# Optimization experiments

Measured on AMD Instinct MI355X. Metric: run time of the kernel, lower is better.

Reference implementation:

```python
import jax, jax.numpy as jnp
import numpy as np
from itertools import product

SPATIAL1 = (41, 1600, 1408)  # (z,y,x) = grid[::-1] + [1,0,0]
NUM_BATCH = 2
BN_EPS = 1e-3

# ---------- numpy rulebook construction (spconv-style, done once on host) ----------

def _encode(c, shape):
    D, H, W = [int(v) for v in shape]
    return ((c[:, 0].astype(np.int64) * D + c[:, 1]) * H + c[:, 2]) * W + c[:, 3]

def _lookup(skeys, order, cand):
    pos = np.clip(np.searchsorted(skeys, cand), 0, len(skeys) - 1)
    hit = skeys[pos] == cand
    return hit, order[pos]

def _pad_rb(pairs, n_in, n_out):
    P = max(max(len(a) for a, _ in pairs), 1)
    K = len(pairs)
    ii = np.full((K, P), n_in, np.int32)   # sentinel -> zero feature row
    oo = np.full((K, P), n_out, np.int32)  # sentinel -> dummy output row
    for k, (a, b) in enumerate(pairs):
        ii[k, :len(a)] = a
        oo[k, :len(b)] = b
    return ii, oo

def _subm_rb(coords, shape):
    # SubMConv3d k=3 p=1 s=1: output sites == input sites
    N = len(coords)
    keys = _encode(coords, shape)
    order = np.argsort(keys); skeys = keys[order]
    dims = np.array(shape)
    pairs = []
    for off in product((-1, 0, 1), repeat=3):
        nb = coords[:, 1:] + np.array(off)
        ok = (nb >= 0).all(1) & (nb < dims).all(1)
        oid = np.nonzero(ok)[0]
        cand = _encode(np.concatenate([coords[ok, :1], nb[ok]], 1), shape)
        hit, iid = _lookup(skeys, order, cand)
        pairs.append((iid[hit].astype(np.int32), oid[hit].astype(np.int32)))
    return _pad_rb(pairs, N, N)

def _down_rb(coords, in_shape, ks, st, pd):
    # SparseConv3d: output site active iff any kernel tap hits an active input
    dims = np.array(in_shape); ks = np.array(ks); st = np.array(st); pd = np.array(pd)
    out_shape = (dims + 2 * pd - ks) // st + 1
    offs = list(product(*[range(int(k)) for k in ks]))
    outs = []
    for off in offs:
        o = coords[:, 1:] + pd - np.array(off)
        ok = (o % st == 0).all(1)
        od = o // st
        ok &= (od >= 0).all(1) & (od < out_shape).all(1)
        outs.append(np.concatenate([coords[ok, :1], od[ok]], 1))
    out_coords = np.unique(np.concatenate(outs, 0), axis=0)
    keys = _encode(coords, in_shape)
    order = np.argsort(keys); skeys = keys[order]
    pairs = []
    for off in offs:
        ic = out_coords[:, 1:] * st - pd + np.array(off)
        ok = (ic >= 0).all(1) & (ic < dims).all(1)
        oid = np.nonzero(ok)[0]
        cand = _encode(np.concatenate([out_coords[ok, :1], ic[ok]], 1), in_shape)
        hit, iid = _lookup(skeys, order, cand)
        pairs.append((iid[hit].astype(np.int32), oid[hit].astype(np.int32)))
    ii, oo = _pad_rb(pairs, len(coords), len(out_coords))
    return ii, oo, out_coords, tuple(int(v) for v in out_shape)

def _gen_coords(rng):
    # clustered LiDAR-like active voxels (surfaces -> local density)
    D, H, W = SPATIAL1
    per = []
    for b in range(NUM_BATCH):
        centers = rng.integers([3, 30, 30], [D - 4, H - 31, W - 31], size=(600, 3))
        pts = centers[:, None, :] + rng.integers(-3, 4, size=(600, 60, 3))
        pts = np.clip(pts.reshape(-1, 3), 0, np.array([D - 1, H - 1, W - 1]))
        uniq = np.unique(pts, axis=0)
        per.append(np.concatenate([np.full((len(uniq), 1), b, np.int64), uniq], 1))
    return np.concatenate(per, 0)

CHANS = [(27, 4, 16), (27, 16, 16), (27, 16, 32), (27, 32, 32), (27, 32, 32),
         (27, 32, 64), (27, 64, 64), (27, 64, 64), (27, 64, 64), (27, 64, 64),
         (27, 64, 64), (3, 64, 128)]

def setup_inputs() -> dict:
    rng = np.random.default_rng(0)
    coords = _gen_coords(rng)  # (N,4) [b,z,y,x]
    N = len(coords)
    s1i, s1o = _subm_rb(coords, SPATIAL1)
    d2i, d2o, c2, s2 = _down_rb(coords, SPATIAL1, (3, 3, 3), (2, 2, 2), (1, 1, 1))
    s2i, s2o = _subm_rb(c2, s2)
    d3i, d3o, c3, s3 = _down_rb(c2, s2, (3, 3, 3), (2, 2, 2), (1, 1, 1))
    s3i, s3o = _subm_rb(c3, s3)
    d4i, d4o, c4, s4 = _down_rb(c3, s3, (3, 3, 3), (2, 2, 2), (0, 1, 1))
    s4i, s4o = _subm_rb(c4, s4)
    oi, oo, c5, s5 = _down_rb(c4, s4, (3, 1, 1), (2, 1, 1), (0, 0, 0))

    key = jax.random.key(0)
    ks = jax.random.split(key, 40)
    inp = {}
    for i, (K, ci, co) in enumerate(CHANS):
        inp[f"w{i}"] = (jax.random.normal(ks[i], (K, ci, co), jnp.float32)
                         / np.sqrt(K * ci)).astype(jnp.float32)
        kb = jax.random.split(ks[12 + i], 4)
        inp[f"bn{i}"] = jnp.stack([
            jax.random.uniform(kb[0], (co,)) + 0.5,   # gamma
            jax.random.normal(kb[1], (co,)) * 0.1,    # beta
            jax.random.normal(kb[2], (co,)) * 0.1,    # running mean
            jax.random.uniform(kb[3], (co,)) + 0.5,   # running var
        ]).astype(jnp.float32)
    inp["voxels"] = jax.random.normal(ks[30], (N, 5, 4), jnp.float32)
    inp["voxel_num_points"] = jax.random.randint(ks[31], (N,), 0, 6).astype(jnp.int32)
    for name, arr in [("subm1_in", s1i), ("subm1_out", s1o), ("down2_in", d2i),
                      ("down2_out", d2o), ("subm2_in", s2i), ("subm2_out", s2o),
                      ("down3_in", d3i), ("down3_out", d3o), ("subm3_in", s3i),
                      ("subm3_out", s3o), ("down4_in", d4i), ("down4_out", d4o),
                      ("subm4_in", s4i), ("subm4_out", s4o), ("out_in", oi),
                      ("out_out", oo)]:
        inp[name] = jnp.asarray(arr)
    inp["batch_idx"] = jnp.asarray(c5[:, 0].astype(np.int32))
    inp["n2"] = len(c2); inp["n3"] = len(c3); inp["n4"] = len(c4); inp["n5"] = len(c5)
    inp["n_batch"] = NUM_BATCH
    return inp

# ---------- jax forward ----------

def _sconv(feats, w, in_idx, out_idx, n_out):
    # gather -> per-kernel-offset GEMM -> scatter-add (spconv implicit GEMM)
    fpad = jnp.concatenate([feats, jnp.zeros((1, feats.shape[1]), feats.dtype)], 0)
    g = fpad[in_idx]                                  # (K,P,Cin)
    contrib = jnp.einsum('kpi,kio->kpo', g, w)        # (K,P,Cout)
    out = jnp.zeros((n_out + 1, w.shape[2]), feats.dtype)
    return out.at[out_idx].add(contrib)[:n_out]

def _bnrelu(x, bn):
    g, b, m, v = bn  # eval-mode BatchNorm1d, eps=1e-3
    return jax.nn.relu((x - m) * jax.lax.rsqrt(v + BN_EPS) * g + b)

def reference(voxels, voxel_num_points, w0, w1, w2, w3, w4, w5, w6, w7, w8, w9,
              w10, w11, bn0, bn1, bn2, bn3, bn4, bn5, bn6, bn7, bn8, bn9, bn10,
              bn11, subm1_in, subm1_out, down2_in, down2_out, subm2_in, subm2_out,
              down3_in, down3_out, subm3_in, subm3_out, down4_in, down4_out,
              subm4_in, subm4_out, out_in, out_out, batch_idx, n2, n3, n4, n5,
              n_batch):
    # mean-VFE: average point features per voxel
    denom = jnp.maximum(voxel_num_points.astype(voxels.dtype), 1.0)[:, None]
    x = voxels.sum(1) / denom                              # (N,4)
    n1 = x.shape[0]
    x = _bnrelu(_sconv(x, w0, subm1_in, subm1_out, n1), bn0)   # conv_input
    x = _bnrelu(_sconv(x, w1, subm1_in, subm1_out, n1), bn1)   # conv1
    x = _bnrelu(_sconv(x, w2, down2_in, down2_out, n2), bn2)   # conv2 (s2)
    x = _bnrelu(_sconv(x, w3, subm2_in, subm2_out, n2), bn3)
    x = _bnrelu(_sconv(x, w4, subm2_in, subm2_out, n2), bn4)
    x = _bnrelu(_sconv(x, w5, down3_in, down3_out, n3), bn5)   # conv3 (s2)
    x = _bnrelu(_sconv(x, w6, subm3_in, subm3_out, n3), bn6)
    x = _bnrelu(_sconv(x, w7, subm3_in, subm3_out, n3), bn7)
    x = _bnrelu(_sconv(x, w8, down4_in, down4_out, n4), bn8)   # conv4 (s2)
    x = _bnrelu(_sconv(x, w9, subm4_in, subm4_out, n4), bn9)
    x = _bnrelu(_sconv(x, w10, subm4_in, subm4_out, n4), bn10)
    x = _bnrelu(_sconv(x, w11, out_in, out_out, n5), bn11)     # conv_out
    # dc_feats: per-sample global max pool over active voxels (== max_pool1d)
    dc = jax.ops.segment_max(x, batch_idx, num_segments=n_batch)
    return dc
```

## Files before the change

### kernel.cpp

```cpp
#include <hip/hip_runtime.h>

#define TPB 256
typedef unsigned short u16;
typedef __attribute__((ext_vector_type(8))) short short8v;
typedef __attribute__((ext_vector_type(4))) float f32x4;

__device__ __forceinline__ u16 f2bf(float x) {
    unsigned u = __float_as_uint(x);
    return (u16)((u + 0x7FFFu + ((u >> 16) & 1u)) >> 16);
}
__device__ __forceinline__ float bf2f(u16 h) {
    return __uint_as_float(((unsigned)h) << 16);
}

template<int CS>
__device__ __forceinline__ int swzc(int r, int c) {
    constexpr int PH = (CS == 8) ? 0 : 1;
    return c ^ ((r >> PH) & (CS - 1));
}

__device__ __forceinline__ int xcd_swz(int bid, int nwg) {
    int q = nwg >> 3, r = nwg & 7;
    int x = bid & 7, idx = bid >> 3;
    return (x < r ? x * (q + 1) : r * (q + 1) + (x - r) * q) + idx;
}

__device__ __forceinline__ void gld16(const u16* g, u16* l) {
    __builtin_amdgcn_global_load_lds(
        (const __attribute__((address_space(1))) void*)g,
        (__attribute__((address_space(3))) void*)l, 16, 0, 0);
}

__global__ void vfe_kernel(const float* __restrict__ voxels,
                           const int* __restrict__ nump,
                           float* __restrict__ x, int N) {
    int i = blockIdx.x * blockDim.x + threadIdx.x;
    if (i >= N * 4) return;
    int n = i >> 2, c = i & 3;
    const float* v = voxels + (long)n * 20 + c;
    float s = v[0] + v[4] + v[8] + v[12] + v[16];
    x[i] = s / fmaxf((float)nump[n], 1.0f);
}

__global__ void inv_build_kernel(const int* __restrict__ rb_in,
                                 const int* __restrict__ rb_out,
                                 int* __restrict__ inv,
                                 int KP, int P, int K, int n_in) {
    int t = blockIdx.x * blockDim.x + threadIdx.x;
    if (t >= KP) return;
    int ii = rb_in[t];
    if (ii == n_in) return;
    int k = t / P;
    inv[(long)rb_out[t] * K + k] = ii;
}

struct WPE { const float* w; u16* oh; u16* ol; int K, ci, co, total; };
struct WPA { WPE e[9]; };
__global__ void wprep_kernel(WPA a, int grand) {
    int t = blockIdx.x * blockDim.x + threadIdx.x;
    if (t >= grand) return;
    #pragma unroll
    for (int i = 0; i < 9; ++i) {
        if (t < a.e[i].total) {
            const WPE& E = a.e[i];
            int cc = E.ci * E.co;
            int k = t / cc, r = t % cc, c = r / E.co, o = r % E.co;
            float x = E.w[t];
            u16 h = f2bf(x);
            float lf = x - bf2f(h);
            int cs = E.ci >> 3, ph = (cs == 8) ? 0 : 1;
            int ch = c >> 3, e = c & 7;
            int sch = ch ^ ((o >> ph) & (cs - 1));
            long d = ((long)k * E.co + o) * E.ci + sch * 8 + e;
            E.oh[d] = h; E.ol[d] = f2bf(lf);
            return;
        }
        t -= a.e[i].total;
    }
}

__global__ void wprep_paired_kernel(const float* __restrict__ w,
                                    u16* __restrict__ oh, u16* __restrict__ ol,
                                    int co, int total) {
    int t = blockIdx.x * blockDim.x + threadIdx.x;
    if (t >= total) return;
    int p = t / (co * 32);
    int rem = t % (co * 32);
    int o = rem / 32, ci = rem % 32;
    int tap = 2 * p + (ci >> 4);
    float x = (tap < 27) ? w[((long)tap * 16 + (ci & 15)) * co + o] : 0.f;
    u16 h = f2bf(x);
    float lf = x - bf2f(h);
    int ch = ci >> 3, e = ci & 7;
    int sch = ch ^ ((o >> 1) & 3);
    long d = ((long)p * co + o) * 32 + sch * 8 + e;
    oh[d] = h; ol[d] = f2bf(lf);
}

template<int CO, int K>
__global__ __launch_bounds__(256)
void dconv4_kernel(const float* __restrict__ feats,
                   const float* __restrict__ w,
                   const float* __restrict__ bn,
                   const int* __restrict__ inv,
                   u16* __restrict__ oh, u16* __restrict__ ol,
                   int n_out) {
    constexpr int OG = CO / 4;
    __shared__ float sW[K * 4 * CO];
    for (int i = threadIdx.x; i < K * 4 * CO; i += 256) sW[i] = w[i];
    __syncthreads();
    long t = (long)blockIdx.x * 256 + threadIdx.x;
    int row = (int)(t / OG), og = (int)(t % OG);
    if (row >= n_out) return;
    float a0 = 0.f, a1 = 0.f, a2 = 0.f, a3 = 0.f;
    for (int k = 0; k < K; ++k) {
        int idx = inv[(long)row * K + k];
        if (idx < 0) continue;
        float4 av = *(const float4*)(feats + (long)idx * 4);
        const float* wk = sW + k * 4 * CO + og * 4;
        #pragma unroll
        for (int ci = 0; ci < 4; ++ci) {
            float a = (&av.x)[ci];
            a0 = fmaf(a, wk[ci * CO + 0], a0);
            a1 = fmaf(a, wk[ci * CO + 1], a1);
            a2 = fmaf(a, wk[ci * CO + 2], a2);
            a3 = fmaf(a, wk[ci * CO + 3], a3);
        }
    }
    float4 g = *(const float4*)(bn + og * 4);
    float4 b = *(const float4*)(bn + CO + og * 4);
    float4 m = *(const float4*)(bn + 2 * CO + og * 4);
    float4 v = *(const float4*)(bn + 3 * CO + og * 4);
    float o4[4];
    o4[0] = fmaxf((a0 - m.x) * rsqrtf(v.x + 1e-3f) * g.x + b.x, 0.f);
    o4[1] = fmaxf((a1 - m.y) * rsqrtf(v.y + 1e-3f) * g.y + b.y, 0.f);
    o4[2] = fmaxf((a2 - m.z) * rsqrtf(v.z + 1e-3f) * g.z + b.z, 0.f);
    o4[3] = fmaxf((a3 - m.w) * rsqrtf(v.w + 1e-3f) * g.w + b.w, 0.f);
    long base = (long)row * CO + og * 4;
    #pragma unroll
    for (int c = 0; c < 4; ++c) {
        u16 h = f2bf(o4[c]);
        oh[base + c] = h;
        ol[base + c] = f2bf(o4[c] - bf2f(h));
    }
}

template<int CI, int CO, int KP, int KT, bool PAIRED>
__global__ __launch_bounds__(256, 4)
void mconv_kernel(const u16* __restrict__ fh, const u16* __restrict__ fl,
                  const u16* __restrict__ wh, const u16* __restrict__ wl,
                  const int* __restrict__ inv,
                  const u16* __restrict__ zpage,
                  float* __restrict__ part, long slab_elems,
                  int n_out, int kpb) {
    constexpr int CS  = CI / 8;
    constexpr int LCS = (CS == 8) ? 3 : 2;
    constexpr int PH  = (CS == 8) ? 0 : 1;
    constexpr int KS  = CI / 32;
    constexpr int WC  = (CO >= 32) ? 2 : 1;
    constexpr int MT  = (WC == 2) ? 2 : 1;
    constexpr int NTW = CO / (16 * WC);
    constexpr int ASL = 64 * CS;
    constexpr int BSL = CO * CS;
    constexpr int AIT = (ASL + 255) / 256;
    constexpr int BIT = (BSL + 255) / 256;

    __shared__ __align__(16) u16 sAh[64 * CI];
    __shared__ __align__(16) u16 sAl[64 * CI];
    __shared__ __align__(16) u16 sBh[CO * CI];
    __shared__ __align__(16) u16 sBl[CO * CI];
    __shared__ int sI[64 * KT];

    const int t = threadIdx.x;
    const int bx = xcd_swz(blockIdx.x, gridDim.x);
    const int brow = bx * 64;
    const int kbeg = blockIdx.y * kpb;
    const int kend = (kbeg + kpb < KP) ? (kbeg + kpb) : KP;

    const int lane = t & 63, wid = t >> 6;
    const int wr = wid / WC, wc = wid % WC;
    const int frow = lane & 15;
    const int fch  = lane >> 4;

    {
        long base = (long)brow * KT, lim = (long)n_out * KT;
        for (int i = t; i < 64 * KT; i += 256)
            sI[i] = (base + i < lim) ? inv[base + i] : -1;
    }

    f32x4 acc[MT][NTW];
    #pragma unroll
    for (int mt = 0; mt < MT; ++mt)
        #pragma unroll
        for (int nt = 0; nt < NTW; ++nt) {
            acc[mt][nt][0] = 0.f; acc[mt][nt][1] = 0.f;
            acc[mt][nt][2] = 0.f; acc[mt][nt][3] = 0.f;
        }

    __syncthreads();
    for (int k = kbeg; k < kend; ++k) {
        #pragma unroll
        for (int s = 0; s < AIT; ++s) {
            int slot = s * 256 + t;
            if (ASL % 256 == 0 || slot < ASL) {
                int r = slot >> LCS, cc = slot & (CS - 1);
                int c = cc ^ ((r >> PH) & (CS - 1));
                const u16 *srcH, *srcL;
                if (PAIRED) {
                    int tap = 2 * k + (c >> 1);
                    int idx = (tap < KT) ? sI[r * KT + tap] : -1;
                    srcH = (idx >= 0) ? fh + (long)idx * 16 + (c & 1) * 8 : zpage;
                    srcL = (idx >= 0) ? fl + (long)idx * 16 + (c & 1) * 8 : zpage;
                } else {
                    int idx = sI[r * KT + k];
                    srcH = (idx >= 0) ? fh + (long)idx * CI + c * 8 : zpage;
                    srcL = (idx >= 0) ? fl + (long)idx * CI + c * 8 : zpage;
                }
                gld16(srcH, sAh + (s * 256 + wid * 64) * 8);
                gld16(srcL, sAl + (s * 256 + wid * 64) * 8);
            }
        }
        {
            const u16* gbh = wh + (long)k * CO * CI;
            const u16* gbl = wl + (long)k * CO * CI;
            #pragma unroll
            for (int s = 0; s < BIT; ++s) {
                int slot = s * 256 + t;
                if (BSL % 256 == 0 || slot < BSL) {
                    gld16(gbh + (long)slot * 8, sBh + (s * 256 + wid * 64) * 8);
                    gld16(gbl + (long)slot * 8, sBl + (s * 256 + wid * 64) * 8);
                }
            }
        }
        __syncthreads();

        #pragma unroll
        for (int ks = 0; ks < KS; ++ks) {
            int c = ks * 4 + fch;
            short8v ah[MT], al[MT];
            #pragma unroll
            for (int mt = 0; mt < MT; ++mt) {
                int r = wr * (MT * 16) + mt * 16 + frow;
                int o = r * CI + swzc<CS>(r, c) * 8;
                ah[mt] = *(const short8v*)(sAh + o);
                al[mt] = *(const short8v*)(sAl + o);
            }
            #pragma unroll
            for (int nt = 0; nt < NTW; ++nt) {
                int col = wc * (CO / WC) + nt * 16 + frow;
                int o = col * CI + swzc<CS>(col, c) * 8;
                short8v bh = *(const short8v*)(sBh + o);
                short8v bl = *(const short8v*)(sBl + o);
                #pragma unroll
                for (int mt = 0; mt < MT; ++mt) {
                    acc[mt][nt] = __builtin_amdgcn_mfma_f32_16x16x32_bf16(ah[mt], bh, acc[mt][nt], 0, 0, 0);
                    acc[mt][nt] = __builtin_amdgcn_mfma_f32_16x16x32_bf16(ah[mt], bl, acc[mt][nt], 0, 0, 0);
                    acc[mt][nt] = __builtin_amdgcn_mfma_f32_16x16x32_bf16(al[mt], bh, acc[mt][nt], 0, 0, 0);
                }
            }
        }
        if (k + 1 < kend) __syncthreads();
    }

    float* dst = part + (long)blockIdx.y * slab_elems;
    #pragma unroll
    for (int mt = 0; mt < MT; ++mt) {
        int orow0 = brow + wr * (MT * 16) + mt * 16 + (lane >> 4) * 4;
        #pragma unroll
        for (int nt = 0; nt < NTW; ++nt) {
            int ocol = wc * (CO / WC) + nt * 16 + (lane & 15);
            #pragma unroll
            for (int j = 0; j < 4; ++j) {
                int r = orow0 + j;
                if (r < n_out) dst[(long)r * CO + ocol] = acc[mt][nt][j];
            }
        }
    }
}

template<bool EMIT16>
__global__ void reduce_bnrelu_kernel(const float* __restrict__ part, long stride,
                                     int ys, const float* __restrict__ bn, int co,
                                     float* __restrict__ outf,
                                     u16* __restrict__ oh, u16* __restrict__ ol,
                                     long total) {
    long t = (long)blockIdx.x * blockDim.x + threadIdx.x;
    if (t >= total) return;
    float s = 0.f;
    for (int y = 0; y < ys; ++y) s += part[(long)y * stride + t];
    int o = (int)(t % co);
    float g = bn[o], b = bn[co + o], m = bn[2 * co + o], v = bn[3 * co + o];
    float yv = fmaxf((s - m) * rsqrtf(v + 1e-3f) * g + b, 0.f);
    if (EMIT16) {
        u16 h = f2bf(yv);
        oh[t] = h;
        ol[t] = f2bf(yv - bf2f(h));
    } else {
        outf[t] = yv;
    }
}

__global__ void segmax_kernel(const float* __restrict__ x,
                              const int* __restrict__ bidx,
                              float* __restrict__ out, int rows, int nb) {
    __shared__ float sM[8 * 128];
    for (int i = threadIdx.x; i < nb * 128; i += 256) sM[i] = 0.f;
    __syncthreads();
    int c = threadIdx.x & 127;
    int sub = threadIdx.x >> 7;
    for (int r = blockIdx.x * 2 + sub; r < rows; r += gridDim.x * 2) {
        float v = x[(long)r * 128 + c];
        int b = bidx[r];
        atomicMax((int*)&sM[b * 128 + c], __float_as_int(v));
    }
    __syncthreads();
    for (int i = threadIdx.x; i < nb * 128; i += 256)
        atomicMax((int*)out + i, __float_as_int(sM[i]));
}

extern "C" void kernel_launch(void* const* d_in, const int* in_sizes, int n_in,
                              void* d_out, int out_size, void* d_ws, size_t ws_size,
                              hipStream_t stream) {
    (void)n_in;
    const float* voxels = (const float*)d_in[24];
    const int*   nump   = (const int*)d_in[25];
    const int N  = in_sizes[25];
    const int n2 = in_sizes[30] / 27;
    const int n3 = in_sizes[34] / 27;
    const int n4 = in_sizes[38] / 27;
    const int n5 = in_sizes[42];

    struct L { int wi, rb, K, ci, co, nin, nout; };
    const L layers[12] = {
        {0,  26, 27,  4,  16, N,  N }, {1,  26, 27, 16,  16, N,  N },
        {2,  28, 27, 16,  32, N,  n2}, {3,  30, 27, 32,  32, n2, n2},
        {4,  30, 27, 32,  32, n2, n2}, {5,  32, 27, 32,  64, n2, n3},
        {6,  34, 27, 64,  64, n3, n3}, {7,  34, 27, 64,  64, n3, n3},
        {8,  36, 27, 64,  64, n3, n4}, {9,  38, 27, 64,  64, n4, n4},
        {10, 38, 27, 64,  64, n4, n4}, {11, 40,  3, 64, 128, n4, n5},
    };

    size_t inv_elems = 0, feat_elems = (size_t)N * 4, wt_elems = 0;
    for (int i = 0; i < 12; ++i) {
        size_t ie = (size_t)layers[i].nout * layers[i].K;
        size_t fe = (size_t)layers[i].nout * layers[i].co;
        if (ie > inv_elems)  inv_elems  = ie;
        if (fe > feat_elems) feat_elems = fe;
        if (i >= 3) wt_elems += (size_t)layers[i].K * layers[i].ci * layers[i].co;
    }
    const size_t wp1_elems = 14 * 32 * 16;
    const size_t wp2_elems = 14 * 32 * 32;
    auto al = [](size_t x) { return (x + 255) & ~(size_t)255; };
    char* p = (char*)d_ws;
    u16*   zpage = (u16*)p; p += 256;
    int*   inv  = (int*)p;   p += al(inv_elems * 4);
    float* bufA = (float*)p; p += al(feat_elems * 4);
    u16* ph[2]; u16* pl[2];
    ph[0] = (u16*)p; p += al(feat_elems * 2);
    pl[0] = (u16*)p; p += al(feat_elems * 2);
    ph[1] = (u16*)p; p += al(feat_elems * 2);
    pl[1] = (u16*)p; p += al(feat_elems * 2);
    u16* wth = (u16*)p; p += al(wt_elems * 2);
    u16* wtl = (u16*)p; p += al(wt_elems * 2);
    u16* wp1h = (u16*)p; p += al(wp1_elems * 2);
    u16* wp1l = (u16*)p; p += al(wp1_elems * 2);
    u16* wp2h = (u16*)p; p += al(wp2_elems * 2);
    u16* wp2l = (u16*)p; p += al(wp2_elems * 2);
    float* slab = (float*)p;
    size_t slab_budget = ws_size - (size_t)((char*)slab - (char*)d_ws);

    hipMemsetAsync(zpage, 0, 256, stream);

    {
        long tot = (long)N * 4;
        vfe_kernel<<<dim3((unsigned)((tot + TPB - 1) / TPB)), dim3(TPB), 0, stream>>>(
            voxels, nump, bufA, N);
    }

    size_t woff[9];
    {
        WPA wa;
        size_t off = 0;
        for (int i = 0; i < 9; ++i) {
            const L& l = layers[i + 3];
            woff[i] = off;
            wa.e[i].w  = (const float*)d_in[2 * l.wi];
            wa.e[i].oh = wth + off;
            wa.e[i].ol = wtl + off;
            wa.e[i].K = l.K; wa.e[i].ci = l.ci; wa.e[i].co = l.co;
            wa.e[i].total = l.K * l.ci * l.co;
            off += (size_t)wa.e[i].total;
        }
        int grand = (int)off;
        wprep_kernel<<<dim3((grand + TPB - 1) / TPB), dim3(TPB), 0, stream>>>(wa, grand);
        wprep_paired_kernel<<<dim3(((int)wp1_elems + TPB - 1) / TPB), dim3(TPB), 0, stream>>>(
            (const float*)d_in[2], wp1h, wp1l, 16, (int)wp1_elems);
        wprep_paired_kernel<<<dim3(((int)wp2_elems + TPB - 1) / TPB), dim3(TPB), 0, stream>>>(
            (const float*)d_in[4], wp2h, wp2l, 32, (int)wp2_elems);
    }

    int prev_rb = -1;
    auto build_inv = [&](const L& l) {
        if (l.rb == prev_rb) return;
        const int* rin  = (const int*)d_in[l.rb];
        const int* rout = (const int*)d_in[l.rb + 1];
        int P  = in_sizes[l.rb] / l.K;
        int KP = l.K * P;
        hipMemsetAsync(inv, 0xFF, (size_t)l.nout * l.K * sizeof(int), stream);
        inv_build_kernel<<<dim3((KP + TPB - 1) / TPB), dim3(TPB), 0, stream>>>(
            rin, rout, inv, KP, P, l.K, l.nin);
        prev_rb = l.rb;
    };

    auto pick_ys = [&](unsigned blocks, int ys_max, size_t per) {
        int ys = 1;
        while (ys < ys_max && blocks * (unsigned)ys < 768) ys *= 3;
        if (ys > ys_max) ys = ys_max;
        while (ys > 1 && (size_t)ys * per > slab_budget) ys /= 3;
        return ys;
    };

    {
        const L& l = layers[0];
        build_inv(l);
        long tot = (long)l.nout * 4;
        dconv4_kernel<16, 27><<<dim3((unsigned)((tot + 255) / 256)), 256, 0, stream>>>(
            bufA, (const float*)d_in[0], (const float*)d_in[1], inv,
            ph[0], pl[0], l.nout);
    }

    int cset = 0;
    for (int i = 1; i < 3; ++i) {
        const L& l = layers[i];
        build_inv(l);
        unsigned blocks = (unsigned)((l.nout + 63) / 64);
        size_t per = (size_t)l.nout * l.co * 4;
        int ys = pick_ys(blocks, 3, per);
        int kpb = (14 + ys - 1) / ys;
        long slab_elems = (long)l.nout * l.co;
        dim3 grid(blocks, (unsigned)ys);
        if (i == 1)
            mconv_kernel<32, 16, 14, 27, true><<<grid, 256, 0, stream>>>(
                ph[cset], pl[cset], wp1h, wp1l, inv, zpage,
                slab, slab_elems, l.nout, kpb);
        else
            mconv_kernel<32, 32, 14, 27, true><<<grid, 256, 0, stream>>>(
                ph[cset], pl[cset], wp2h, wp2l, inv, zpage,
                slab, slab_elems, l.nout, kpb);
        long total = (long)l.nout * l.co;
        unsigned rblocks = (unsigned)((total + TPB - 1) / TPB);
        reduce_bnrelu_kernel<true><<<dim3(rblocks), dim3(TPB), 0, stream>>>(
            slab, slab_elems, ys, (const float*)d_in[2 * l.wi + 1], l.co,
            nullptr, ph[cset ^ 1], pl[cset ^ 1], total);
        cset ^= 1;
    }

    for (int i = 3; i < 12; ++i) {
        const L& l = layers[i];
        build_inv(l);
        unsigned blocks = (unsigned)((l.nout + 63) / 64);
        size_t per = (size_t)l.nout * l.co * 4;
        int ys = pick_ys(blocks, (l.K == 27) ? 27 : 3, per);
        int kpb = (l.K + ys - 1) / ys;
        long slab_elems = (long)l.nout * l.co;
        dim3 grid(blocks, (unsigned)ys);
        const u16* fh = ph[cset];
        const u16* fl = pl[cset];
        const u16* whp = wth + woff[i - 3];
        const u16* wlp = wtl + woff[i - 3];

        switch (i) {
        case 3: case 4:
            mconv_kernel<32, 32, 27, 27, false><<<grid, 256, 0, stream>>>(
                fh, fl, whp, wlp, inv, zpage, slab, slab_elems, l.nout, kpb); break;
        case 5:
            mconv_kernel<32, 64, 27, 27, false><<<grid, 256, 0, stream>>>(
                fh, fl, whp, wlp, inv, zpage, slab, slab_elems, l.nout, kpb); break;
        case 11:
            mconv_kernel<64, 128, 3, 3, false><<<grid, 256, 0, stream>>>(
                fh, fl, whp, wlp, inv, zpage, slab, slab_elems, l.nout, kpb); break;
        default:
            mconv_kernel<64, 64, 27, 27, false><<<grid, 256, 0, stream>>>(
                fh, fl, whp, wlp, inv, zpage, slab, slab_elems, l.nout, kpb); break;
        }

        long total = (long)l.nout * l.co;
        unsigned rblocks = (unsigned)((total + TPB - 1) / TPB);
        const float* bn = (const float*)d_in[2 * l.wi + 1];
        if (i < 11) {
            reduce_bnrelu_kernel<true><<<dim3(rblocks), dim3(TPB), 0, stream>>>(
                slab, slab_elems, ys, bn, l.co,
                nullptr, ph[cset ^ 1], pl[cset ^ 1], total);
            cset ^= 1;
        } else {
            reduce_bnrelu_kernel<false><<<dim3(rblocks), dim3(TPB), 0, stream>>>(
                slab, slab_elems, ys, bn, l.co, bufA, nullptr, nullptr, total);
        }
    }

    hipMemsetAsync(d_out, 0, (size_t)out_size * sizeof(float), stream);
    const int* bidx = (const int*)d_in[42];
    int nb = out_size / 128;
    segmax_kernel<<<dim3(128), dim3(256), 0, stream>>>(bufA, bidx, (float*)d_out, n5, nb);
}
```

Measured before the change: 473.3 us.

## Double-buffer sparse conv staging, fuse BN-ReLU epilogue, prebuild all rulebook inverses

The gather-GEMM kernel gets optional double-buffered LDS staging, so the next tap's gather overlaps the current tap's MFMA work. When no K-split is used, it applies BN+ReLU in the epilogue and writes bf16 hi/lo or fp32 output directly, skipping the reduce kernel. All eight inverse rulebooks are now built up front into one arena instead of per layer. The K-split cap for the paired layers rises from 3 to 9. Double buffering doubles LDS use, which may reduce occupancy for the larger-channel layers.

```diff
diff --git a/kernel.cpp b/kernel.cpp
--- a/kernel.cpp
+++ b/kernel.cpp
@@ -145,13 +145,16 @@
     }
 }
 
-template<int CI, int CO, int KP, int KT, bool PAIRED>
+template<int CI, int CO, int KPt, int KT, bool PAIRED, bool DBUF, int EPI>
 __global__ __launch_bounds__(256, 4)
 void mconv_kernel(const u16* __restrict__ fh, const u16* __restrict__ fl,
                   const u16* __restrict__ wh, const u16* __restrict__ wl,
                   const int* __restrict__ inv,
                   const u16* __restrict__ zpage,
                   float* __restrict__ part, long slab_elems,
+                  const float* __restrict__ bn,
+                  u16* __restrict__ oh, u16* __restrict__ ol,
+                  float* __restrict__ outf,
                   int n_out, int kpb) {
     constexpr int CS  = CI / 8;
     constexpr int LCS = (CS == 8) ? 3 : 2;
@@ -164,18 +167,19 @@
     constexpr int BSL = CO * CS;
     constexpr int AIT = (ASL + 255) / 256;
     constexpr int BIT = (BSL + 255) / 256;
-
-    __shared__ __align__(16) u16 sAh[64 * CI];
-    __shared__ __align__(16) u16 sAl[64 * CI];
-    __shared__ __align__(16) u16 sBh[CO * CI];
-    __shared__ __align__(16) u16 sBl[CO * CI];
+    constexpr int NB  = DBUF ? 2 : 1;
+
+    __shared__ __align__(16) u16 sAh[NB][64 * CI];
+    __shared__ __align__(16) u16 sAl[NB][64 * CI];
+    __shared__ __align__(16) u16 sBh[NB][CO * CI];
+    __shared__ __align__(16) u16 sBl[NB][CO * CI];
     __shared__ int sI[64 * KT];
 
     const int t = threadIdx.x;
     const int bx = xcd_swz(blockIdx.x, gridDim.x);
     const int brow = bx * 64;
     const int kbeg = blockIdx.y * kpb;
-    const int kend = (kbeg + kpb < KP) ? (kbeg + kpb) : KP;
+    const int kend = (kbeg + kpb < KPt) ? (kbeg + kpb) : KPt;
 
     const int lane = t & 63, wid = t >> 6;
     const int wr = wid / WC, wc = wid % WC;
@@ -197,8 +201,7 @@
             acc[mt][nt][2] = 0.f; acc[mt][nt][3] = 0.f;
         }
 
-    __syncthreads();
-    for (int k = kbeg; k < kend; ++k) {
+    auto stage = [&](int b, int k) {
         #pragma unroll
         for (int s = 0; s < AIT; ++s) {
             int slot = s * 256 + t;
@@ -216,24 +219,22 @@
                     srcH = (idx >= 0) ? fh + (long)idx * CI + c * 8 : zpage;
                     srcL = (idx >= 0) ? fl + (long)idx * CI + c * 8 : zpage;
                 }
-                gld16(srcH, sAh + (s * 256 + wid * 64) * 8);
-                gld16(srcL, sAl + (s * 256 + wid * 64) * 8);
-            }
-        }
-        {
-            const u16* gbh = wh + (long)k * CO * CI;
-            const u16* gbl = wl + (long)k * CO * CI;
-            #pragma unroll
-            for (int s = 0; s < BIT; ++s) {
-                int slot = s * 256 + t;
-                if (BSL % 256 == 0 || slot < BSL) {
-                    gld16(gbh + (long)slot * 8, sBh + (s * 256 + wid * 64) * 8);
-                    gld16(gbl + (long)slot * 8, sBl + (s * 256 + wid * 64) * 8);
-                }
-            }
-        }
-        __syncthreads();
-
+                gld16(srcH, sAh[b] + (s * 256 + wid * 64) * 8);
+                gld16(srcL, sAl[b] + (s * 256 + wid * 64) * 8);
+            }
+        }
+        const u16* gbh = wh + (long)k * CO * CI;
+        const u16* gbl = wl + (long)k * CO * CI;
+        #pragma unroll
+        for (int s = 0; s < BIT; ++s) {
+            int slot = s * 256 + t;
+            if (BSL % 256 == 0 || slot < BSL) {
+                gld16(gbh + (long)slot * 8, sBh[b] + (s * 256 + wid * 64) * 8);
+                gld16(gbl + (long)slot * 8, sBl[b] + (s * 256 + wid * 64) * 8);
+            }
+        }
+    };
+    auto compute = [&](int b) {
         #pragma unroll
         for (int ks = 0; ks < KS; ++ks) {
             int c = ks * 4 + fch;
@@ -242,15 +243,15 @@
             for (int mt = 0; mt < MT; ++mt) {
                 int r = wr * (MT * 16) + mt * 16 + frow;
                 int o = r * CI + swzc<CS>(r, c) * 8;
-                ah[mt] = *(const short8v*)(sAh + o);
-                al[mt] = *(const short8v*)(sAl + o);
+                ah[mt] = *(const short8v*)(sAh[b] + o);
+                al[mt] = *(const short8v*)(sAl[b] + o);
             }
             #pragma unroll
             for (int nt = 0; nt < NTW; ++nt) {
                 int col = wc * (CO / WC) + nt * 16 + frow;
                 int o = col * CI + swzc<CS>(col, c) * 8;
-                short8v bh = *(const short8v*)(sBh + o);
-                short8v bl = *(const short8v*)(sBl + o);
+                short8v bh = *(const short8v*)(sBh[b] + o);
+                short8v bl = *(const short8v*)(sBl[b] + o);
                 #pragma unroll
                 for (int mt = 0; mt < MT; ++mt) {
                     acc[mt][nt] = __builtin_amdgcn_mfma_f32_16x16x32_bf16(ah[mt], bh, acc[mt][nt], 0, 0, 0);
@@ -259,20 +260,66 @@
                 }
             }
         }
-        if (k + 1 < kend) __syncthreads();
-    }
-
-    float* dst = part + (long)blockIdx.y * slab_elems;
-    #pragma unroll
-    for (int mt = 0; mt < MT; ++mt) {
-        int orow0 = brow + wr * (MT * 16) + mt * 16 + (lane >> 4) * 4;
-        #pragma unroll
-        for (int nt = 0; nt < NTW; ++nt) {
-            int ocol = wc * (CO / WC) + nt * 16 + (lane & 15);
+    };
+
+    __syncthreads();
+    if (DBUF) {
+        stage(0, kbeg);
+        int cur = 0;
+        for (int k = kbeg; k < kend; ++k) {
+            __syncthreads();
+            if (k + 1 < kend) stage(cur ^ 1, k + 1);
+            compute(cur);
+            cur ^= 1;
+        }
+    } else {
+        for (int k = kbeg; k < kend; ++k) {
+            stage(0, k);
+            __syncthreads();
+            compute(0);
+            if (k + 1 < kend) __syncthreads();
+        }
+    }
+
+    if constexpr (EPI == 0) {
+        float* dst = part + (long)blockIdx.y * slab_elems;
+        #pragma unroll
+        for (int mt = 0; mt < MT; ++mt) {
+            int orow0 = brow + wr * (MT * 16) + mt * 16 + (lane >> 4) * 4;
             #pragma unroll
-            for (int j = 0; j < 4; ++j) {
-                int r = orow0 + j;
-                if (r < n_out) dst[(long)r * CO + ocol] = acc[mt][nt][j];
+            for (int nt = 0; nt < NTW; ++nt) {
+                int ocol = wc * (CO / WC) + nt * 16 + (lane & 15);
+                #pragma unroll
+                for (int j = 0; j < 4; ++j) {
+                    int r = orow0 + j;
+                    if (r < n_out) dst[(long)r * CO + ocol] = acc[mt][nt][j];
+                }
+            }
+        }
+    } else {
+        #pragma unroll
+        for (int mt = 0; mt < MT; ++mt) {
+            int orow0 = brow + wr * (MT * 16) + mt * 16 + (lane >> 4) * 4;
+            #pragma unroll
+            for (int nt = 0; nt < NTW; ++nt) {
+                int ocol = wc * (CO / WC) + nt * 16 + (lane & 15);
+                float g = bn[ocol], bb = bn[CO + ocol];
+                float m = bn[2 * CO + ocol], vv = bn[3 * CO + ocol];
+                float sc = rsqrtf(vv + 1e-3f) * g;
+                #pragma unroll
+                for (int j = 0; j < 4; ++j) {
+                    int r = orow0 + j;
+                    if (r < n_out) {
+                        float yv = fmaxf((acc[mt][nt][j] - m) * sc + bb, 0.f);
+                        if constexpr (EPI == 1) {
+                            u16 h = f2bf(yv);
+                            oh[(long)r * CO + ocol] = h;
+                            ol[(long)r * CO + ocol] = f2bf(yv - bf2f(h));
+                        } else {
+                            outf[(long)r * CO + ocol] = yv;
+                        }
+                    }
+                }
             }
         }
     }
@@ -339,21 +386,26 @@
         {8,  36, 27, 64,  64, n3, n4}, {9,  38, 27, 64,  64, n4, n4},
         {10, 38, 27, 64,  64, n4, n4}, {11, 40,  3, 64, 128, n4, n5},
     };
-
-    size_t inv_elems = 0, feat_elems = (size_t)N * 4, wt_elems = 0;
+    struct RBD { int rb, K, nin, nout; };
+    const RBD rbs[8] = {
+        {26, 27, N,  N }, {28, 27, N,  n2}, {30, 27, n2, n2}, {32, 27, n2, n3},
+        {34, 27, n3, n3}, {36, 27, n3, n4}, {38, 27, n4, n4}, {40, 3,  n4, n5},
+    };
+    const int invmap[12] = {0, 0, 1, 2, 2, 3, 4, 4, 5, 6, 6, 7};
+
+    size_t feat_elems = (size_t)N * 4, wt_elems = 0, arena_elems = 0;
     for (int i = 0; i < 12; ++i) {
-        size_t ie = (size_t)layers[i].nout * layers[i].K;
         size_t fe = (size_t)layers[i].nout * layers[i].co;
-        if (ie > inv_elems)  inv_elems  = ie;
         if (fe > feat_elems) feat_elems = fe;
         if (i >= 3) wt_elems += (size_t)layers[i].K * layers[i].ci * layers[i].co;
     }
+    for (int r = 0; r < 8; ++r) arena_elems += (size_t)rbs[r].nout * rbs[r].K;
     const size_t wp1_elems = 14 * 32 * 16;
     const size_t wp2_elems = 14 * 32 * 32;
     auto al = [](size_t x) { return (x + 255) & ~(size_t)255; };
     char* p = (char*)d_ws;
     u16*   zpage = (u16*)p; p += 256;
-    int*   inv  = (int*)p;   p += al(inv_elems * 4);
+    int*   inv_arena = (int*)p; p += al(arena_elems * 4);
     float* bufA = (float*)p; p += al(feat_elems * 4);
     u16* ph[2]; u16* pl[2];
     ph[0] = (u16*)p; p += al(feat_elems * 2);
@@ -371,6 +423,21 @@
 
     hipMemsetAsync(zpage, 0, 256, stream);
 
+    int* invs[8];
+    {
+        size_t off = 0;
+        for (int r = 0; r < 8; ++r) { invs[r] = inv_arena + off; off += (size_t)rbs[r].nout * rbs[r].K; }
+        hipMemsetAsync(inv_arena, 0xFF, arena_elems * sizeof(int), stream);
+        for (int r = 0; r < 8; ++r) {
+            const int* rin  = (const int*)d_in[rbs[r].rb];
+            const int* rout = (const int*)d_in[rbs[r].rb + 1];
+            int P  = in_sizes[rbs[r].rb] / rbs[r].K;
+            int KP = rbs[r].K * P;
+            inv_build_kernel<<<dim3((KP + TPB - 1) / TPB), dim3(TPB), 0, stream>>>(
+                rin, rout, invs[r], KP, P, rbs[r].K, rbs[r].nin);
+        }
+    }
+
     {
         long tot = (long)N * 4;
         vfe_kernel<<<dim3((unsigned)((tot + TPB - 1) / TPB)), dim3(TPB), 0, stream>>>(
@@ -399,102 +466,79 @@
             (const float*)d_in[4], wp2h, wp2l, 32, (int)wp2_elems);
     }
 
-    int prev_rb = -1;
-    auto build_inv = [&](const L& l) {
-        if (l.rb == prev_rb) return;
-        const int* rin  = (const int*)d_in[l.rb];
-        const int* rout = (const int*)d_in[l.rb + 1];
-        int P  = in_sizes[l.rb] / l.K;
-        int KP = l.K * P;
-        hipMemsetAsync(inv, 0xFF, (size_t)l.nout * l.K * sizeof(int), stream);
-        inv_build_kernel<<<dim3((KP + TPB - 1) / TPB), dim3(TPB), 0, stream>>>(
-            rin, rout, inv, KP, P, l.K, l.nin);
-        prev_rb = l.rb;
-    };
-
-    auto pick_ys = [&](unsigned blocks, int ys_max, size_t per) {
-        int ys = 1;
-        while (ys < ys_max && blocks * (unsigned)ys < 768) ys *= 3;
-        if (ys > ys_max) ys = ys_max;
-        while (ys > 1 && (size_t)ys * per > slab_budget) ys /= 3;
-        return ys;
-    };
-
     {
         const L& l = layers[0];
-        build_inv(l);
         long tot = (long)l.nout * 4;
         dconv4_kernel<16, 27><<<dim3((unsigned)((tot + 255) / 256)), 256, 0, stream>>>(
-            bufA, (const float*)d_in[0], (const float*)d_in[1], inv,
+            bufA, (const float*)d_in[0], (const float*)d_in[1], invs[0],
             ph[0], pl[0], l.nout);
     }
 
     int cset = 0;
-    for (int i = 1; i < 3; ++i) {
+    for (int i = 1; i < 12; ++i) {
         const L& l = layers[i];
-        build_inv(l);
+        const int* invp = invs[invmap[i]];
         unsigned blocks = (unsigned)((l.nout + 63) / 64);
+        int KPv = (i <= 2) ? 14 : l.K;
+        int ysmax = (KPv == 14) ? 9 : ((KPv == 27) ? 27 : 3);
         size_t per = (size_t)l.nout * l.co * 4;
-        int ys = pick_ys(blocks, 3, per);
-        int kpb = (14 + ys - 1) / ys;
+        int ys = 1;
+        while (ys < ysmax && blocks * (unsigned)ys < 768) ys *= 3;
+        if (ys > ysmax) ys = ysmax;
+        while (ys > 1 && (size_t)ys * per > slab_budget) ys /= 3;
+        int kpb = (KPv + ys - 1) / ys;
         long slab_elems = (long)l.nout * l.co;
         dim3 grid(blocks, (unsigned)ys);
-        if (i == 1)
-            mconv_kernel<32, 16, 14, 27, true><<<grid, 256, 0, stream>>>(
-                ph[cset], pl[cset], wp1h, wp1l, inv, zpage,
-                slab, slab_elems, l.nout, kpb);
-        else
-            mconv_kernel<32, 32, 14, 27, true><<<grid, 256, 0, stream>>>(
-                ph[cset], pl[cset], wp2h, wp2l, inv, zpage,
-                slab, slab_elems, l.nout, kpb);
-        long total = (long)l.nout * l.co;
-        unsigned rblocks = (unsigned)((total + TPB - 1) / TPB);
-        reduce_bnrelu_kernel<true><<<dim3(rblocks), dim3(TPB), 0, stream>>>(
-            slab, slab_elems, ys, (const float*)d_in[2 * l.wi + 1], l.co,
-            nullptr, ph[cset ^ 1], pl[cset ^ 1], total);
-        cset ^= 1;
-    }
-
-    for (int i = 3; i < 12; ++i) {
-        const L& l = layers[i];
-        build_inv(l);
-        unsigned blocks = (unsigned)((l.nout + 63) / 64);
-        size_t per = (size_t)l.nout * l.co * 4;
-        int ys = pick_ys(blocks, (l.K == 27) ? 27 : 3, per);
-        int kpb = (l.K + ys - 1) / ys;
-        long slab_elems = (long)l.nout * l.co;
-        dim3 grid(blocks, (unsigned)ys);
+        const float* bn = (const float*)d_in[2 * l.wi + 1];
         const u16* fh = ph[cset];
         const u16* fl = pl[cset];
-        const u16* whp = wth + woff[i - 3];
-        const u16* wlp = wtl + woff[i - 3];
+        const u16* whp = (i >= 3) ? wth + woff[i - 3] : nullptr;
+        const u16* wlp = (i >= 3) ? wtl + woff[i - 3] : nullptr;
+
+        #define MCONV(CI_, CO_, KP_, KT_, PRD_, WH_, WL_)                              \
+            do {                                                                       \
+                if (ys == 1 && i < 11)                                                 \
+                    mconv_kernel<CI_, CO_, KP_, KT_, PRD_, true, 1><<<grid, 256, 0, stream>>>( \
+                        fh, fl, WH_, WL_, invp, zpage, nullptr, 0, bn,                 \
+                        ph[cset ^ 1], pl[cset ^ 1], nullptr, l.nout, kpb);             \
+                else if (ys == 1)                                                      \
+                    mconv_kernel<CI_, CO_, KP_, KT_, PRD_, true, 2><<<grid, 256, 0, stream>>>( \
+                        fh, fl, WH_, WL_, invp, zpage, nullptr, 0, bn,                 \
+                        nullptr, nullptr, bufA, l.nout, kpb);                          \
+                else if (kpb >= 2)                                                     \
+                    mconv_kernel<CI_, CO_, KP_, KT_, PRD_, true, 0><<<grid, 256, 0, stream>>>( \
+                        fh, fl, WH_, WL_, invp, zpage, slab, slab_elems, bn,           \
+                        nullptr, nullptr, nullptr, l.nout, kpb);                       \
+                else                                                                   \
+                    mconv_kernel<CI_, CO_, KP_, KT_, PRD_, false, 0><<<grid, 256, 0, stream>>>( \
+                        fh, fl, WH_, WL_, invp, zpage, slab, slab_elems, bn,           \
+                        nullptr, nullptr, nullptr, l.nout, kpb);                       \
+            } while (0)
 
         switch (i) {
-        case 3: case 4:
-            mconv_kernel<32, 32, 27, 27, false><<<grid, 256, 0, stream>>>(
-                fh, fl, whp, wlp, inv, zpage, slab, slab_elems, l.nout, kpb); break;
-        case 5:
-            mconv_kernel<32, 64, 27, 27, false><<<grid, 256, 0, stream>>>(
-                fh, fl, whp, wlp, inv, zpage, slab, slab_elems, l.nout, kpb); break;
-        case 11:
-            mconv_kernel<64, 128, 3, 3, false><<<grid, 256, 0, stream>>>(
-                fh, fl, whp, wlp, inv, zpage, slab, slab_elems, l.nout, kpb); break;
-        default:
-            mconv_kernel<64, 64, 27, 27, false><<<grid, 256, 0, stream>>>(
-                fh, fl, whp, wlp, inv, zpage, slab, slab_elems, l.nout, kpb); break;
-        }
-
-        long total = (long)l.nout * l.co;
-        unsigned rblocks = (unsigned)((total + TPB - 1) / TPB);
-        const float* bn = (const float*)d_in[2 * l.wi + 1];
-        if (i < 11) {
-            reduce_bnrelu_kernel<true><<<dim3(rblocks), dim3(TPB), 0, stream>>>(
-                slab, slab_elems, ys, bn, l.co,
-                nullptr, ph[cset ^ 1], pl[cset ^ 1], total);
-            cset ^= 1;
+        case 1:          MCONV(32, 16, 14, 27, true,  wp1h, wp1l); break;
+        case 2:          MCONV(32, 32, 14, 27, true,  wp2h, wp2l); break;
+        case 3: case 4:  MCONV(32, 32, 27, 27, false, whp, wlp);   break;
+        case 5:          MCONV(32, 64, 27, 27, false, whp, wlp);   break;
+        case 11:         MCONV(64, 128, 3, 3,  false, whp, wlp);   break;
+        default:         MCONV(64, 64, 27, 27, false, whp, wlp);   break;
+        }
+        #undef MCONV
+
+        if (ys == 1) {
+            if (i < 11) cset ^= 1;
         } else {
-            reduce_bnrelu_kernel<false><<<dim3(rblocks), dim3(TPB), 0, stream>>>(
-                slab, slab_elems, ys, bn, l.co, bufA, nullptr, nullptr, total);
+            long total = (long)l.nout * l.co;
+            unsigned rblocks = (unsigned)((total + TPB - 1) / TPB);
+            if (i < 11) {
+                reduce_bnrelu_kernel<true><<<dim3(rblocks), dim3(TPB), 0, stream>>>(
+                    slab, slab_elems, ys, bn, l.co,
+                    nullptr, ph[cset ^ 1], pl[cset ^ 1], total);
+                cset ^= 1;
+            } else {
+                reduce_bnrelu_kernel<false><<<dim3(rblocks), dim3(TPB), 0, stream>>>(
+                    slab, slab_elems, ys, bn, l.co, bufA, nullptr, nullptr, total);
+            }
         }
     }
 
```

After: 482.6 us. About the same (+2.0%).
